# Kernel tuning notes

Hardware: AMD Instinct MI355X
Metric: run time of the kernel (lower is better)

## Reference

```python
import jax, jax.numpy as jnp
import numpy as np

N_NODES = 50000
N_EDGES = 800000


def _sage(x, src, dst, Wl, Wr, b, n):
    # PyG SAGEConv: lin_l(mean aggr of neighbors) + lin_r(x) (+ bias in lin_l)
    agg = jax.ops.segment_sum(x[src], dst, num_segments=n)
    cnt = jax.ops.segment_sum(jnp.ones((src.shape[0],), x.dtype), dst, num_segments=n)
    mean = agg / jnp.maximum(cnt, 1.0)[:, None]
    return mean @ Wl + x @ Wr + b


def _gat(x, src, dst, W, att_src, att_dst, b, n):
    H, C = att_src.shape
    h = (x @ W).reshape(n, H, C)                      # [N,H,C]
    a_s = jnp.sum(h * att_src, axis=-1)               # [N,H]
    a_d = jnp.sum(h * att_dst, axis=-1)               # [N,H]
    e = jax.nn.leaky_relu(a_s[src] + a_d[dst], 0.2)   # [E,H]
    m = jax.ops.segment_max(e, dst, num_segments=n)   # per-dst softmax (stable)
    ex = jnp.exp(e - m[dst])
    s = jax.ops.segment_sum(ex, dst, num_segments=n)
    alpha = ex / (s[dst] + 1e-16)                     # [E,H]
    out = jax.ops.segment_sum(h[src] * alpha[:, :, None], dst, num_segments=n)
    return out.reshape(n, H * C) + b


def setup_inputs() -> dict:
    key = jax.random.key(0)
    ks = jax.random.split(key, 16)
    F_IN, H1, GH, HEADS, H2, NC = 20, 256, 32, 4, 256, 5
    GOUT = GH * HEADS
    sc = 0.05
    return {
        "x": jax.random.normal(ks[0], (N_NODES, F_IN), jnp.float32),
        "edge_index": jax.random.randint(ks[1], (2, N_EDGES), 0, N_NODES, jnp.int32),
        "sage1_Wl": jax.random.normal(ks[2], (F_IN, H1), jnp.float32) * sc,
        "sage1_Wr": jax.random.normal(ks[3], (F_IN, H1), jnp.float32) * sc,
        "sage1_b": jnp.zeros((H1,), jnp.float32),
        "gat_W": jax.random.normal(ks[4], (H1, GOUT), jnp.float32) * sc,
        "gat_att_src": jax.random.normal(ks[5], (HEADS, GH), jnp.float32) * sc,
        "gat_att_dst": jax.random.normal(ks[6], (HEADS, GH), jnp.float32) * sc,
        "gat_b": jnp.zeros((GOUT,), jnp.float32),
        "sage2_Wl": jax.random.normal(ks[7], (GOUT, H2), jnp.float32) * sc,
        "sage2_Wr": jax.random.normal(ks[8], (GOUT, H2), jnp.float32) * sc,
        "sage2_b": jnp.zeros((H2,), jnp.float32),
        "cls_W": jax.random.normal(ks[9], (H2, NC), jnp.float32) * sc,
        "cls_b": jnp.zeros((NC,), jnp.float32),
    }


def reference(x, edge_index, sage1_Wl, sage1_Wr, sage1_b, gat_W, gat_att_src,
              gat_att_dst, gat_b, sage2_Wl, sage2_Wr, sage2_b, cls_W, cls_b):
    n = x.shape[0]
    src, dst = edge_index[0], edge_index[1]
    h = jax.nn.relu(_sage(x, src, dst, sage1_Wl, sage1_Wr, sage1_b, n))
    h = jax.nn.elu(_gat(h, src, dst, gat_W, gat_att_src, gat_att_dst, gat_b, n))
    h = jax.nn.relu(_sage(h, src, dst, sage2_Wl, sage2_Wr, sage2_b, n))
    return h @ cls_W + cls_b
```

## Files before the change

### kernel.cpp

```cpp
#include <hip/hip_runtime.h>
#include <math.h>

#define N_NODES 50000
#define N_EDGES 800000
#define TPB 256
#define NCHUNK ((N_NODES + 255) / 256)

typedef short s16x8 __attribute__((ext_vector_type(8)));
typedef float f32x4 __attribute__((ext_vector_type(4)));

__device__ __forceinline__ unsigned short f2bf(float f) {
    unsigned u = __float_as_uint(f);
    u += 0x7fffu + ((u >> 16) & 1u);
    return (unsigned short)(u >> 16);
}
__device__ __forceinline__ float bf2f(unsigned short h) {
    return __uint_as_float(((unsigned)h) << 16);
}

__global__ void wt_all_k(const float* __restrict__ s1Wl, const float* __restrict__ s1Wr,
                         const float* __restrict__ gW, const float* __restrict__ s2Wl,
                         const float* __restrict__ s2Wr, unsigned short* __restrict__ Wt1,
                         unsigned short* __restrict__ Wt2, unsigned short* __restrict__ Wt3) {
    int idx = blockIdx.x * TPB + threadIdx.x;
    if (idx < 16384) {
        int n = idx >> 6, k = idx & 63;
        float v = 0.f;
        if (k < 20) v = s1Wl[k * 256 + n];
        else if (k < 40) v = s1Wr[(k - 20) * 256 + n];
        Wt1[idx] = f2bf(v);
    } else if (idx < 49152) {
        int j = idx - 16384;
        int n = j >> 8, k = j & 255;
        Wt2[j] = f2bf(gW[(size_t)k * 128 + n]);
    } else if (idx < 114688) {
        int j = idx - 49152;
        int n = j >> 8, k = j & 255;
        float v = (k < 128) ? s2Wl[(size_t)k * 256 + n] : s2Wr[(size_t)(k - 128) * 256 + n];
        Wt3[j] = f2bf(v);
    }
}

template<int ACT, int OBF>
__global__ void gemm_mfma(const float* __restrict__ A1, int K1,
                          const float* __restrict__ A2, int K2,
                          const unsigned short* __restrict__ Wt, int Kp,
                          const float* __restrict__ bias,
                          float* __restrict__ out, unsigned short* __restrict__ outb,
                          int NO) {
    constexpr int BM = 128, BK = 32, LDP = 40;
    __shared__ unsigned short sA[BM * LDP];
    __shared__ unsigned short sB[128 * LDP];
    const int K = K1 + K2;
    const int T = Kp / BK;
    const int tid = threadIdx.x;
    const int lane = tid & 63, wid = tid >> 6;
    const int wr = wid >> 1, wc = wid & 1;
    const int row0 = blockIdx.y * BM, col0 = blockIdx.x * 128;
    const int l15 = lane & 15, l4 = lane >> 4;
    f32x4 acc[4][4] = {};

    for (int t = 0; t < T; ++t) {
        __syncthreads();
#pragma unroll
        for (int j = 0; j < 4; ++j) {
            int e = tid + j * 256;
            int r = e >> 3, k4 = e & 7;
            int kg = t * BK + k4 * 4, mg = row0 + r;
            float4 v = {0.f, 0.f, 0.f, 0.f};
            if (mg < N_NODES) {
                if (kg < K1)     v = *(const float4*)&A1[(size_t)mg * K1 + kg];
                else if (kg < K) v = *(const float4*)&A2[(size_t)mg * K2 + (kg - K1)];
            }
            ushort4 b;
            b.x = f2bf(v.x); b.y = f2bf(v.y); b.z = f2bf(v.z); b.w = f2bf(v.w);
            *(ushort4*)&sA[r * LDP + k4 * 4] = b;
        }
#pragma unroll
        for (int j = 0; j < 2; ++j) {
            int e = tid + j * 256;
            int n = e >> 2, k8 = e & 3;
            int4 v = *(const int4*)&Wt[(size_t)(col0 + n) * Kp + t * BK + k8 * 8];
            *(int4*)&sB[n * LDP + k8 * 8] = v;
        }
        __syncthreads();
        s16x8 af[4], bfr[4];
#pragma unroll
        for (int i = 0; i < 4; ++i) {
            af[i]  = *(const s16x8*)&sA[(wr * 64 + i * 16 + l15) * LDP + l4 * 8];
            bfr[i] = *(const s16x8*)&sB[(wc * 64 + i * 16 + l15) * LDP + l4 * 8];
        }
#pragma unroll
        for (int mi = 0; mi < 4; ++mi)
#pragma unroll
            for (int ni = 0; ni < 4; ++ni)
                acc[mi][ni] = __builtin_amdgcn_mfma_f32_16x16x32_bf16(
                    af[mi], bfr[ni], acc[mi][ni], 0, 0, 0);
    }
#pragma unroll
    for (int mi = 0; mi < 4; ++mi) {
#pragma unroll
        for (int ni = 0; ni < 4; ++ni) {
            int col = col0 + wc * 64 + ni * 16 + l15;
            float bb = bias ? bias[col] : 0.f;
#pragma unroll
            for (int r = 0; r < 4; ++r) {
                int row = row0 + wr * 64 + mi * 16 + l4 * 4 + r;
                if (row < N_NODES) {
                    float v = acc[mi][ni][r] + bb;
                    if (ACT) v = fmaxf(v, 0.f);
                    if (OBF) outb[(size_t)row * NO + col] = f2bf(v);
                    else     out[(size_t)row * NO + col] = v;
                }
            }
        }
    }
}

template<int ACT, int OBF>
__global__ void gemm_mfma_bf(const unsigned short* __restrict__ A1, int K1,
                             const unsigned short* __restrict__ A2, int K2,
                             const unsigned short* __restrict__ Wt, int Kp,
                             const float* __restrict__ bias,
                             float* __restrict__ out, unsigned short* __restrict__ outb,
                             int NO) {
    constexpr int BM = 128, BK = 32, LDP = 40;
    __shared__ unsigned short sA[BM * LDP];
    __shared__ unsigned short sB[128 * LDP];
    const int T = Kp / BK;
    const int tid = threadIdx.x;
    const int lane = tid & 63, wid = tid >> 6;
    const int wr = wid >> 1, wc = wid & 1;
    const int row0 = blockIdx.y * BM, col0 = blockIdx.x * 128;
    const int l15 = lane & 15, l4 = lane >> 4;
    f32x4 acc[4][4] = {};

    for (int t = 0; t < T; ++t) {
        __syncthreads();
#pragma unroll
        for (int j = 0; j < 2; ++j) {
            int e = tid + j * 256;
            int r = e >> 2, k8 = e & 3;
            int kg = t * BK + k8 * 8, mg = row0 + r;
            int4 v = {0, 0, 0, 0};
            if (mg < N_NODES) {
                if (kg < K1) v = *(const int4*)&A1[(size_t)mg * K1 + kg];
                else         v = *(const int4*)&A2[(size_t)mg * K2 + (kg - K1)];
            }
            *(int4*)&sA[r * LDP + k8 * 8] = v;
        }
#pragma unroll
        for (int j = 0; j < 2; ++j) {
            int e = tid + j * 256;
            int n = e >> 2, k8 = e & 3;
            int4 v = *(const int4*)&Wt[(size_t)(col0 + n) * Kp + t * BK + k8 * 8];
            *(int4*)&sB[n * LDP + k8 * 8] = v;
        }
        __syncthreads();
        s16x8 af[4], bfr[4];
#pragma unroll
        for (int i = 0; i < 4; ++i) {
            af[i]  = *(const s16x8*)&sA[(wr * 64 + i * 16 + l15) * LDP + l4 * 8];
            bfr[i] = *(const s16x8*)&sB[(wc * 64 + i * 16 + l15) * LDP + l4 * 8];
        }
#pragma unroll
        for (int mi = 0; mi < 4; ++mi)
#pragma unroll
            for (int ni = 0; ni < 4; ++ni)
                acc[mi][ni] = __builtin_amdgcn_mfma_f32_16x16x32_bf16(
                    af[mi], bfr[ni], acc[mi][ni], 0, 0, 0);
    }
#pragma unroll
    for (int mi = 0; mi < 4; ++mi) {
#pragma unroll
        for (int ni = 0; ni < 4; ++ni) {
            int col = col0 + wc * 64 + ni * 16 + l15;
            float bb = bias ? bias[col] : 0.f;
#pragma unroll
            for (int r = 0; r < 4; ++r) {
                int row = row0 + wr * 64 + mi * 16 + l4 * 4 + r;
                if (row < N_NODES) {
                    float v = acc[mi][ni][r] + bb;
                    if (ACT) v = fmaxf(v, 0.f);
                    if (OBF) outb[(size_t)row * NO + col] = f2bf(v);
                    else     out[(size_t)row * NO + col] = v;
                }
            }
        }
    }
}

__global__ void hist_k(const int* __restrict__ dst, int* __restrict__ deg) {
    int e = blockIdx.x * TPB + threadIdx.x;
    if (e < N_EDGES) atomicAdd(&deg[dst[e]], 1);
}

__global__ void scan1_k(const int* __restrict__ deg, int* __restrict__ rowptr,
                        int* __restrict__ bsum) {
    __shared__ int tmp[256];
    int tid = threadIdx.x;
    int idx = blockIdx.x * 256 + tid;
    int v = (idx < N_NODES) ? deg[idx] : 0;
    tmp[tid] = v;
    __syncthreads();
    for (int off = 1; off < 256; off <<= 1) {
        int t = (tid >= off) ? tmp[tid - off] : 0;
        __syncthreads();
        tmp[tid] += t;
        __syncthreads();
    }
    if (idx < N_NODES) rowptr[idx] = tmp[tid] - v;
    if (tid == 255) bsum[blockIdx.x] = tmp[255];
}

__global__ void scan2_k(int* __restrict__ bsum) {
    __shared__ int tmp[256];
    int tid = threadIdx.x;
    int v = (tid < NCHUNK) ? bsum[tid] : 0;
    tmp[tid] = v;
    __syncthreads();
    for (int off = 1; off < 256; off <<= 1) {
        int t = (tid >= off) ? tmp[tid - off] : 0;
        __syncthreads();
        tmp[tid] += t;
        __syncthreads();
    }
    if (tid < NCHUNK) bsum[tid] = tmp[tid] - v;
}

__global__ void scan3_k(int* __restrict__ rowptr, const int* __restrict__ bsum) {
    int idx = blockIdx.x * 256 + threadIdx.x;
    if (idx < N_NODES) rowptr[idx] += bsum[blockIdx.x];
    if (idx == 0) rowptr[N_NODES] = N_EDGES;
}

__global__ void fill_k(const int* __restrict__ src, const int* __restrict__ dst,
                       const int* __restrict__ rowptr, int* __restrict__ deg,
                       int* __restrict__ csr_src) {
    int e = blockIdx.x * TPB + threadIdx.x;
    if (e >= N_EDGES) return;
    int d = dst[e];
    int r = atomicSub(&deg[d], 1) - 1;
    csr_src[rowptr[d] + r] = src[e];
}

__global__ void gm20_k(const int* __restrict__ rowptr, const int* __restrict__ csr_src,
                       const float* __restrict__ feat, float* __restrict__ out) {
    int tid = threadIdx.x;
    int n = blockIdx.x * 8 + (tid >> 5);
    int c = tid & 31;
    if (n >= N_NODES || c >= 20) return;
    int e0 = rowptr[n], e1 = rowptr[n + 1];
    float acc = 0.f;
    int e = e0;
    for (; e + 1 < e1; e += 2) {
        acc += feat[(size_t)csr_src[e] * 20 + c] + feat[(size_t)csr_src[e + 1] * 20 + c];
    }
    if (e < e1) acc += feat[(size_t)csr_src[e] * 20 + c];
    out[(size_t)n * 20 + c] = acc / fmaxf((float)(e1 - e0), 1.0f);
}

__global__ void gather_mean_bf(const int* __restrict__ rowptr, const int* __restrict__ csr_src,
                               const unsigned short* __restrict__ featb,
                               unsigned short* __restrict__ outb) {
    int tid = threadIdx.x;
    int n = blockIdx.x * 8 + (tid >> 5);
    int c = tid & 31;
    int e0 = rowptr[n], e1 = rowptr[n + 1];
    float4 acc = {0.f, 0.f, 0.f, 0.f};
    int e = e0;
    for (; e + 3 < e1; e += 4) {
        int s0 = csr_src[e], s1 = csr_src[e + 1], s2 = csr_src[e + 2], s3 = csr_src[e + 3];
        ushort4 u0 = *(const ushort4*)&featb[(size_t)s0 * 128 + c * 4];
        ushort4 u1 = *(const ushort4*)&featb[(size_t)s1 * 128 + c * 4];
        ushort4 u2 = *(const ushort4*)&featb[(size_t)s2 * 128 + c * 4];
        ushort4 u3 = *(const ushort4*)&featb[(size_t)s3 * 128 + c * 4];
        acc.x += (bf2f(u0.x) + bf2f(u1.x)) + (bf2f(u2.x) + bf2f(u3.x));
        acc.y += (bf2f(u0.y) + bf2f(u1.y)) + (bf2f(u2.y) + bf2f(u3.y));
        acc.z += (bf2f(u0.z) + bf2f(u1.z)) + (bf2f(u2.z) + bf2f(u3.z));
        acc.w += (bf2f(u0.w) + bf2f(u1.w)) + (bf2f(u2.w) + bf2f(u3.w));
    }
    for (; e < e1; ++e) {
        ushort4 u = *(const ushort4*)&featb[(size_t)csr_src[e] * 128 + c * 4];
        acc.x += bf2f(u.x); acc.y += bf2f(u.y); acc.z += bf2f(u.z); acc.w += bf2f(u.w);
    }
    float inv = 1.0f / fmaxf((float)(e1 - e0), 1.0f);
    ushort4 o;
    o.x = f2bf(acc.x * inv); o.y = f2bf(acc.y * inv);
    o.z = f2bf(acc.z * inv); o.w = f2bf(acc.w * inv);
    *(ushort4*)&outb[(size_t)n * 128 + c * 4] = o;
}

__global__ void att_scores_bf(const unsigned short* __restrict__ hb,
                              const float* __restrict__ att_src,
                              const float* __restrict__ att_dst,
                              float* __restrict__ as_, float* __restrict__ ad_) {
    int idx = blockIdx.x * TPB + threadIdx.x;
    if (idx >= N_NODES * 4) return;
    int n = idx >> 2, hd = idx & 3;
    const unsigned short* row = hb + (size_t)n * 128 + hd * 32;
    float sa = 0.f, sd = 0.f;
#pragma unroll
    for (int c4 = 0; c4 < 8; ++c4) {
        ushort4 u = *(const ushort4*)&row[c4 * 4];
        const float* asr = &att_src[hd * 32 + c4 * 4];
        const float* adr = &att_dst[hd * 32 + c4 * 4];
        sa = fmaf(bf2f(u.x), asr[0], sa); sd = fmaf(bf2f(u.x), adr[0], sd);
        sa = fmaf(bf2f(u.y), asr[1], sa); sd = fmaf(bf2f(u.y), adr[1], sd);
        sa = fmaf(bf2f(u.z), asr[2], sa); sd = fmaf(bf2f(u.z), adr[2], sd);
        sa = fmaf(bf2f(u.w), asr[3], sa); sd = fmaf(bf2f(u.w), adr[3], sd);
    }
    as_[idx] = sa;
    ad_[idx] = sd;
}

__global__ void gat_gather_bf(const int* __restrict__ rowptr, const int* __restrict__ csr_src,
                              const unsigned short* __restrict__ hb,
                              const float* __restrict__ as_, const float* __restrict__ ad_,
                              const float* __restrict__ gb,
                              unsigned short* __restrict__ outb) {
    int tid = threadIdx.x;
    int n = blockIdx.x * 8 + (tid >> 5);
    int c = tid & 31;
    int hd = c >> 3;
    int e0 = rowptr[n], e1 = rowptr[n + 1];
    float ad = ad_[n * 4 + hd];
    float m = -INFINITY, s = 0.f;
    float4 acc = {0.f, 0.f, 0.f, 0.f};
    int e = e0;
    for (; e + 3 < e1; e += 4) {
        int s0 = csr_src[e], s1 = csr_src[e + 1], s2 = csr_src[e + 2], s3 = csr_src[e + 3];
        float a0 = as_[s0 * 4 + hd] + ad;
        float a1 = as_[s1 * 4 + hd] + ad;
        float a2 = as_[s2 * 4 + hd] + ad;
        float a3 = as_[s3 * 4 + hd] + ad;
        a0 = a0 >= 0.f ? a0 : 0.2f * a0;
        a1 = a1 >= 0.f ? a1 : 0.2f * a1;
        a2 = a2 >= 0.f ? a2 : 0.2f * a2;
        a3 = a3 >= 0.f ? a3 : 0.2f * a3;
        float pm = fmaxf(fmaxf(a0, a1), fmaxf(a2, a3));
        if (pm > m) {
            float sc = __expf(m - pm);
            s *= sc; acc.x *= sc; acc.y *= sc; acc.z *= sc; acc.w *= sc;
            m = pm;
        }
        float ex0 = __expf(a0 - m), ex1 = __expf(a1 - m);
        float ex2 = __expf(a2 - m), ex3 = __expf(a3 - m);
        s += (ex0 + ex1) + (ex2 + ex3);
        ushort4 u0 = *(const ushort4*)&hb[(size_t)s0 * 128 + c * 4];
        ushort4 u1 = *(const ushort4*)&hb[(size_t)s1 * 128 + c * 4];
        ushort4 u2 = *(const ushort4*)&hb[(size_t)s2 * 128 + c * 4];
        ushort4 u3 = *(const ushort4*)&hb[(size_t)s3 * 128 + c * 4];
        acc.x = fmaf(bf2f(u0.x), ex0, acc.x); acc.y = fmaf(bf2f(u0.y), ex0, acc.y);
        acc.z = fmaf(bf2f(u0.z), ex0, acc.z); acc.w = fmaf(bf2f(u0.w), ex0, acc.w);
        acc.x = fmaf(bf2f(u1.x), ex1, acc.x); acc.y = fmaf(bf2f(u1.y), ex1, acc.y);
        acc.z = fmaf(bf2f(u1.z), ex1, acc.z); acc.w = fmaf(bf2f(u1.w), ex1, acc.w);
        acc.x = fmaf(bf2f(u2.x), ex2, acc.x); acc.y = fmaf(bf2f(u2.y), ex2, acc.y);
        acc.z = fmaf(bf2f(u2.z), ex2, acc.z); acc.w = fmaf(bf2f(u2.w), ex2, acc.w);
        acc.x = fmaf(bf2f(u3.x), ex3, acc.x); acc.y = fmaf(bf2f(u3.y), ex3, acc.y);
        acc.z = fmaf(bf2f(u3.z), ex3, acc.z); acc.w = fmaf(bf2f(u3.w), ex3, acc.w);
    }
    for (; e < e1; ++e) {
        int s0 = csr_src[e];
        float a = as_[s0 * 4 + hd] + ad;
        a = a >= 0.f ? a : 0.2f * a;
        if (a > m) {
            float sc = __expf(m - a);
            s *= sc; acc.x *= sc; acc.y *= sc; acc.z *= sc; acc.w *= sc;
            m = a;
        }
        float ex = __expf(a - m);
        s += ex;
        ushort4 u = *(const ushort4*)&hb[(size_t)s0 * 128 + c * 4];
        acc.x = fmaf(bf2f(u.x), ex, acc.x); acc.y = fmaf(bf2f(u.y), ex, acc.y);
        acc.z = fmaf(bf2f(u.z), ex, acc.z); acc.w = fmaf(bf2f(u.w), ex, acc.w);
    }
    float inv = 1.0f / (s + 1e-16f);
    float rx = acc.x * inv + gb[c * 4 + 0];
    float ry = acc.y * inv + gb[c * 4 + 1];
    float rz = acc.z * inv + gb[c * 4 + 2];
    float rw = acc.w * inv + gb[c * 4 + 3];
    rx = rx > 0.f ? rx : expm1f(rx);
    ry = ry > 0.f ? ry : expm1f(ry);
    rz = rz > 0.f ? rz : expm1f(rz);
    rw = rw > 0.f ? rw : expm1f(rw);
    ushort4 o;
    o.x = f2bf(rx); o.y = f2bf(ry); o.z = f2bf(rz); o.w = f2bf(rw);
    *(ushort4*)&outb[(size_t)n * 128 + c * 4] = o;
}

__global__ void cls_k(const float* __restrict__ h, const float* __restrict__ W,
                      const float* __restrict__ b, float* __restrict__ out) {
    __shared__ float sW[256 * 5];
    for (int i = threadIdx.x; i < 1280; i += TPB) sW[i] = W[i];
    __syncthreads();
    int n = blockIdx.x * TPB + threadIdx.x;
    if (n >= N_NODES) return;
    const float4* row = (const float4*)(h + (size_t)n * 256);
    float acc[5] = {0.f, 0.f, 0.f, 0.f, 0.f};
    for (int k4 = 0; k4 < 64; ++k4) {
        float4 v = row[k4];
        const float* w = &sW[k4 * 4 * 5];
#pragma unroll
        for (int c = 0; c < 5; ++c) acc[c] = fmaf(v.x, w[c], acc[c]);
#pragma unroll
        for (int c = 0; c < 5; ++c) acc[c] = fmaf(v.y, w[5 + c], acc[c]);
#pragma unroll
        for (int c = 0; c < 5; ++c) acc[c] = fmaf(v.z, w[10 + c], acc[c]);
#pragma unroll
        for (int c = 0; c < 5; ++c) acc[c] = fmaf(v.w, w[15 + c], acc[c]);
    }
#pragma unroll
    for (int c = 0; c < 5; ++c) out[(size_t)n * 5 + c] = acc[c] + b[c];
}

extern "C" void kernel_launch(void* const* d_in, const int* in_sizes, int n_in,
                              void* d_out, int out_size, void* d_ws, size_t ws_size,
                              hipStream_t stream) {
    const float* x    = (const float*)d_in[0];
    const int*   ei   = (const int*)d_in[1];
    const float* s1Wl = (const float*)d_in[2];
    const float* s1Wr = (const float*)d_in[3];
    const float* s1b  = (const float*)d_in[4];
    const float* gW   = (const float*)d_in[5];
    const float* gas  = (const float*)d_in[6];
    const float* gad  = (const float*)d_in[7];
    const float* gb   = (const float*)d_in[8];
    const float* s2Wl = (const float*)d_in[9];
    const float* s2Wr = (const float*)d_in[10];
    const float* s2b  = (const float*)d_in[11];
    const float* clsW = (const float*)d_in[12];
    const float* clsb = (const float*)d_in[13];
    float* out = (float*)d_out;
    const int* src = ei;
    const int* dst = ei + N_EDGES;

    float* ws  = (float*)d_ws;
    float* A    = ws;
    float* M20  = A + (size_t)N_NODES * 256;
    float* as_  = M20 + (size_t)N_NODES * 20;
    float* ad_  = as_ + N_NODES * 4;
    int* deg     = (int*)(ad_ + N_NODES * 4);
    int* bsum    = deg + N_NODES;
    int* rowptr  = bsum + 256;
    int* csr_src = rowptr + N_NODES + 1;
    unsigned short* Wt1 = (unsigned short*)(csr_src + N_EDGES);
    unsigned short* Wt2 = Wt1 + 256 * 64;
    unsigned short* Wt3 = Wt2 + 128 * 256;
    unsigned short* Ab  = Wt3 + 256 * 256;
    unsigned short* Cb  = Ab + (size_t)N_NODES * 256;
    unsigned short* Db  = Cb + (size_t)N_NODES * 128;
    unsigned short* Mb  = Db + (size_t)N_NODES * 128;

    const int MB = (N_NODES + 127) / 128;

    wt_all_k<<<(114688 + TPB - 1) / TPB, TPB, 0, stream>>>(s1Wl, s1Wr, gW, s2Wl, s2Wr,
                                                           Wt1, Wt2, Wt3);

    hipMemsetAsync(deg, 0, N_NODES * sizeof(int), stream);
    hist_k<<<(N_EDGES + TPB - 1) / TPB, TPB, 0, stream>>>(dst, deg);
    scan1_k<<<NCHUNK, 256, 0, stream>>>(deg, rowptr, bsum);
    scan2_k<<<1, 256, 0, stream>>>(bsum);
    scan3_k<<<NCHUNK, 256, 0, stream>>>(rowptr, bsum);
    fill_k<<<(N_EDGES + TPB - 1) / TPB, TPB, 0, stream>>>(src, dst, rowptr, deg, csr_src);

    gm20_k<<<(N_NODES + 7) / 8, 256, 0, stream>>>(rowptr, csr_src, x, M20);
    gemm_mfma<1, 1><<<dim3(2, MB), 256, 0, stream>>>(M20, 20, x, 20, Wt1, 64, s1b,
                                                     nullptr, Ab, 256);

    gemm_mfma_bf<0, 1><<<dim3(1, MB), 256, 0, stream>>>(Ab, 256, nullptr, 0, Wt2, 256,
                                                        nullptr, nullptr, Cb, 128);
    att_scores_bf<<<(N_NODES * 4 + TPB - 1) / TPB, TPB, 0, stream>>>(Cb, gas, gad, as_, ad_);
    gat_gather_bf<<<N_NODES / 8, 256, 0, stream>>>(rowptr, csr_src, Cb, as_, ad_, gb, Db);

    gather_mean_bf<<<N_NODES / 8, 256, 0, stream>>>(rowptr, csr_src, Db, Mb);
    gemm_mfma_bf<1, 0><<<dim3(2, MB), 256, 0, stream>>>(Mb, 128, Db, 128, Wt3, 256, s2b,
                                                        A, nullptr, 256);

    cls_k<<<(N_NODES + TPB - 1) / TPB, TPB, 0, stream>>>(A, clsW, clsb, out);
}
```

Baseline: 296.0 us.

## Fuse classifier into final GEMM epilogue, widen gather batches, fold deg memset

The classifier matmul is folded into the epilogue of the last SAGE GEMM. Each column block reduces its ReLU outputs against the class weights in registers and shared memory, writes per-block partials, and a small combine kernel adds the bias. This removes the fp32 N×256 intermediate write and its re-read. The GAT gather now loads 8 edges per iteration, with lanes cooperatively computing scores and broadcasting them by shuffles. The mean gather is unrolled to 8 edges, and zeroing of deg moves into the weight-transpose kernel so the memset call goes away.

After: 299.2 us. No clear change (+1.1%).

```diff
diff --git a/kernel.cpp b/kernel.cpp
--- a/kernel.cpp
+++ b/kernel.cpp
@@ -21,8 +21,10 @@
 __global__ void wt_all_k(const float* __restrict__ s1Wl, const float* __restrict__ s1Wr,
                          const float* __restrict__ gW, const float* __restrict__ s2Wl,
                          const float* __restrict__ s2Wr, unsigned short* __restrict__ Wt1,
-                         unsigned short* __restrict__ Wt2, unsigned short* __restrict__ Wt3) {
+                         unsigned short* __restrict__ Wt2, unsigned short* __restrict__ Wt3,
+                         int* __restrict__ deg) {
     int idx = blockIdx.x * TPB + threadIdx.x;
+    if (idx < N_NODES) deg[idx] = 0;
     if (idx < 16384) {
         int n = idx >> 6, k = idx & 63;
         float v = 0.f;
@@ -41,13 +43,12 @@
     }
 }
 
-template<int ACT, int OBF>
+template<int ACT>
 __global__ void gemm_mfma(const float* __restrict__ A1, int K1,
                           const float* __restrict__ A2, int K2,
                           const unsigned short* __restrict__ Wt, int Kp,
                           const float* __restrict__ bias,
-                          float* __restrict__ out, unsigned short* __restrict__ outb,
-                          int NO) {
+                          unsigned short* __restrict__ outb, int NO) {
     constexpr int BM = 128, BK = 32, LDP = 40;
     __shared__ unsigned short sA[BM * LDP];
     __shared__ unsigned short sB[128 * LDP];
@@ -109,21 +110,20 @@
                 if (row < N_NODES) {
                     float v = acc[mi][ni][r] + bb;
                     if (ACT) v = fmaxf(v, 0.f);
-                    if (OBF) outb[(size_t)row * NO + col] = f2bf(v);
-                    else     out[(size_t)row * NO + col] = v;
+                    outb[(size_t)row * NO + col] = f2bf(v);
                 }
             }
         }
     }
 }
 
-template<int ACT, int OBF>
+template<int ACT, int CLS>
 __global__ void gemm_mfma_bf(const unsigned short* __restrict__ A1, int K1,
                              const unsigned short* __restrict__ A2, int K2,
                              const unsigned short* __restrict__ Wt, int Kp,
                              const float* __restrict__ bias,
-                             float* __restrict__ out, unsigned short* __restrict__ outb,
-                             int NO) {
+                             unsigned short* __restrict__ outb, int NO,
+                             const float* __restrict__ clsW, float* __restrict__ pp) {
     constexpr int BM = 128, BK = 32, LDP = 40;
     __shared__ unsigned short sA[BM * LDP];
     __shared__ unsigned short sB[128 * LDP];
@@ -170,24 +170,81 @@
                 acc[mi][ni] = __builtin_amdgcn_mfma_f32_16x16x32_bf16(
                     af[mi], bfr[ni], acc[mi][ni], 0, 0, 0);
     }
-#pragma unroll
-    for (int mi = 0; mi < 4; ++mi) {
-#pragma unroll
-        for (int ni = 0; ni < 4; ++ni) {
-            int col = col0 + wc * 64 + ni * 16 + l15;
-            float bb = bias ? bias[col] : 0.f;
-#pragma unroll
-            for (int r = 0; r < 4; ++r) {
-                int row = row0 + wr * 64 + mi * 16 + l4 * 4 + r;
-                if (row < N_NODES) {
-                    float v = acc[mi][ni][r] + bb;
-                    if (ACT) v = fmaxf(v, 0.f);
-                    if (OBF) outb[(size_t)row * NO + col] = f2bf(v);
-                    else     out[(size_t)row * NO + col] = v;
+
+    if (CLS == 0) {
+#pragma unroll
+        for (int mi = 0; mi < 4; ++mi) {
+#pragma unroll
+            for (int ni = 0; ni < 4; ++ni) {
+                int col = col0 + wc * 64 + ni * 16 + l15;
+                float bb = bias ? bias[col] : 0.f;
+#pragma unroll
+                for (int r = 0; r < 4; ++r) {
+                    int row = row0 + wr * 64 + mi * 16 + l4 * 4 + r;
+                    if (row < N_NODES) {
+                        float v = acc[mi][ni][r] + bb;
+                        if (ACT) v = fmaxf(v, 0.f);
+                        outb[(size_t)row * NO + col] = f2bf(v);
+                    }
                 }
             }
         }
-    }
+    } else {
+        __syncthreads();
+        float* sClsW = (float*)sA;
+        float* cp    = (float*)sB;
+        for (int i = tid; i < 640; i += 256)
+            sClsW[i] = clsW[(size_t)(col0 + i / 5) * 5 + (i % 5)];
+        __syncthreads();
+        float bcol[4];
+#pragma unroll
+        for (int ni = 0; ni < 4; ++ni)
+            bcol[ni] = bias[col0 + wc * 64 + ni * 16 + l15];
+#pragma unroll
+        for (int mi = 0; mi < 4; ++mi) {
+#pragma unroll
+            for (int r = 0; r < 4; ++r) {
+                float p0 = 0.f, p1 = 0.f, p2 = 0.f, p3 = 0.f, p4 = 0.f;
+#pragma unroll
+                for (int ni = 0; ni < 4; ++ni) {
+                    float v = fmaxf(acc[mi][ni][r] + bcol[ni], 0.f);
+                    const float* w = &sClsW[(wc * 64 + ni * 16 + l15) * 5];
+                    p0 = fmaf(v, w[0], p0); p1 = fmaf(v, w[1], p1);
+                    p2 = fmaf(v, w[2], p2); p3 = fmaf(v, w[3], p3);
+                    p4 = fmaf(v, w[4], p4);
+                }
+#pragma unroll
+                for (int msk = 1; msk < 16; msk <<= 1) {
+                    p0 += __shfl_xor(p0, msk, 16);
+                    p1 += __shfl_xor(p1, msk, 16);
+                    p2 += __shfl_xor(p2, msk, 16);
+                    p3 += __shfl_xor(p3, msk, 16);
+                    p4 += __shfl_xor(p4, msk, 16);
+                }
+                if (l15 == 0) {
+                    int rr = wr * 64 + mi * 16 + l4 * 4 + r;
+                    float* d = &cp[(wc * 128 + rr) * 5];
+                    d[0] = p0; d[1] = p1; d[2] = p2; d[3] = p3; d[4] = p4;
+                }
+            }
+        }
+        __syncthreads();
+        for (int i = tid; i < 640; i += 256) {
+            int rr = i / 5, cc = i - rr * 5;
+            int row = row0 + rr;
+            if (row < N_NODES)
+                pp[(size_t)blockIdx.x * ((size_t)N_NODES * 5) + (size_t)row * 5 + cc]
+                    = cp[rr * 5 + cc] + cp[(128 + rr) * 5 + cc];
+        }
+    }
+}
+
+__global__ void combine_k(const float* __restrict__ pp, const float* __restrict__ clsb,
+                          float* __restrict__ out) {
+    int idx = blockIdx.x * TPB + threadIdx.x;
+    if (idx >= N_NODES * 5) return;
+    int c = idx % 5;
+    out[idx] = pp[idx] + pp[(size_t)N_NODES * 5 + idx] + clsb[c];
 }
 
 __global__ void hist_k(const int* __restrict__ dst, int* __restrict__ deg) {
@@ -269,16 +326,16 @@
     int e0 = rowptr[n], e1 = rowptr[n + 1];
     float4 acc = {0.f, 0.f, 0.f, 0.f};
     int e = e0;
-    for (; e + 3 < e1; e += 4) {
-        int s0 = csr_src[e], s1 = csr_src[e + 1], s2 = csr_src[e + 2], s3 = csr_src[e + 3];
-        ushort4 u0 = *(const ushort4*)&featb[(size_t)s0 * 128 + c * 4];
-        ushort4 u1 = *(const ushort4*)&featb[(size_t)s1 * 128 + c * 4];
-        ushort4 u2 = *(const ushort4*)&featb[(size_t)s2 * 128 + c * 4];
-        ushort4 u3 = *(const ushort4*)&featb[(size_t)s3 * 128 + c * 4];
-        acc.x += (bf2f(u0.x) + bf2f(u1.x)) + (bf2f(u2.x) + bf2f(u3.x));
-        acc.y += (bf2f(u0.y) + bf2f(u1.y)) + (bf2f(u2.y) + bf2f(u3.y));
-        acc.z += (bf2f(u0.z) + bf2f(u1.z)) + (bf2f(u2.z) + bf2f(u3.z));
-        acc.w += (bf2f(u0.w) + bf2f(u1.w)) + (bf2f(u2.w) + bf2f(u3.w));
+    for (; e + 7 < e1; e += 8) {
+        ushort4 u[8];
+#pragma unroll
+        for (int j = 0; j < 8; ++j)
+            u[j] = *(const ushort4*)&featb[(size_t)csr_src[e + j] * 128 + c * 4];
+#pragma unroll
+        for (int j = 0; j < 8; ++j) {
+            acc.x += bf2f(u[j].x); acc.y += bf2f(u[j].y);
+            acc.z += bf2f(u[j].z); acc.w += bf2f(u[j].w);
+        }
     }
     for (; e < e1; ++e) {
         ushort4 u = *(const ushort4*)&featb[(size_t)csr_src[e] * 128 + c * 4];
@@ -323,42 +380,47 @@
     int n = blockIdx.x * 8 + (tid >> 5);
     int c = tid & 31;
     int hd = c >> 3;
+    int q = c & 7;
     int e0 = rowptr[n], e1 = rowptr[n + 1];
     float ad = ad_[n * 4 + hd];
     float m = -INFINITY, s = 0.f;
     float4 acc = {0.f, 0.f, 0.f, 0.f};
     int e = e0;
-    for (; e + 3 < e1; e += 4) {
-        int s0 = csr_src[e], s1 = csr_src[e + 1], s2 = csr_src[e + 2], s3 = csr_src[e + 3];
-        float a0 = as_[s0 * 4 + hd] + ad;
-        float a1 = as_[s1 * 4 + hd] + ad;
-        float a2 = as_[s2 * 4 + hd] + ad;
-        float a3 = as_[s3 * 4 + hd] + ad;
-        a0 = a0 >= 0.f ? a0 : 0.2f * a0;
-        a1 = a1 >= 0.f ? a1 : 0.2f * a1;
-        a2 = a2 >= 0.f ? a2 : 0.2f * a2;
-        a3 = a3 >= 0.f ? a3 : 0.2f * a3;
-        float pm = fmaxf(fmaxf(a0, a1), fmaxf(a2, a3));
+    for (; e + 7 < e1; e += 8) {
+        int sq = csr_src[e + q];
+        float aq = as_[sq * 4 + hd] + ad;
+        aq = aq >= 0.f ? aq : 0.2f * aq;
+        float pm = aq;
+        pm = fmaxf(pm, __shfl_xor(pm, 1, 8));
+        pm = fmaxf(pm, __shfl_xor(pm, 2, 8));
+        pm = fmaxf(pm, __shfl_xor(pm, 4, 8));
         if (pm > m) {
             float sc = __expf(m - pm);
             s *= sc; acc.x *= sc; acc.y *= sc; acc.z *= sc; acc.w *= sc;
             m = pm;
         }
-        float ex0 = __expf(a0 - m), ex1 = __expf(a1 - m);
-        float ex2 = __expf(a2 - m), ex3 = __expf(a3 - m);
-        s += (ex0 + ex1) + (ex2 + ex3);
-        ushort4 u0 = *(const ushort4*)&hb[(size_t)s0 * 128 + c * 4];
-        ushort4 u1 = *(const ushort4*)&hb[(size_t)s1 * 128 + c * 4];
-        ushort4 u2 = *(const ushort4*)&hb[(size_t)s2 * 128 + c * 4];
-        ushort4 u3 = *(const ushort4*)&hb[(size_t)s3 * 128 + c * 4];
-        acc.x = fmaf(bf2f(u0.x), ex0, acc.x); acc.y = fmaf(bf2f(u0.y), ex0, acc.y);
-        acc.z = fmaf(bf2f(u0.z), ex0, acc.z); acc.w = fmaf(bf2f(u0.w), ex0, acc.w);
-        acc.x = fmaf(bf2f(u1.x), ex1, acc.x); acc.y = fmaf(bf2f(u1.y), ex1, acc.y);
-        acc.z = fmaf(bf2f(u1.z), ex1, acc.z); acc.w = fmaf(bf2f(u1.w), ex1, acc.w);
-        acc.x = fmaf(bf2f(u2.x), ex2, acc.x); acc.y = fmaf(bf2f(u2.y), ex2, acc.y);
-        acc.z = fmaf(bf2f(u2.z), ex2, acc.z); acc.w = fmaf(bf2f(u2.w), ex2, acc.w);
-        acc.x = fmaf(bf2f(u3.x), ex3, acc.x); acc.y = fmaf(bf2f(u3.y), ex3, acc.y);
-        acc.z = fmaf(bf2f(u3.z), ex3, acc.z); acc.w = fmaf(bf2f(u3.w), ex3, acc.w);
+        float exq = __expf(aq - m);
+        float exs[8];
+        int   sj[8];
+#pragma unroll
+        for (int j = 0; j < 8; ++j) {
+            exs[j] = __shfl(exq, j, 8);
+            sj[j]  = __shfl(sq, j, 8);
+        }
+        s += ((exs[0] + exs[1]) + (exs[2] + exs[3]))
+           + ((exs[4] + exs[5]) + (exs[6] + exs[7]));
+        ushort4 u[8];
+#pragma unroll
+        for (int j = 0; j < 8; ++j)
+            u[j] = *(const ushort4*)&hb[(size_t)sj[j] * 128 + c * 4];
+#pragma unroll
+        for (int j = 0; j < 8; ++j) {
+            float ex = exs[j];
+            acc.x = fmaf(bf2f(u[j].x), ex, acc.x);
+            acc.y = fmaf(bf2f(u[j].y), ex, acc.y);
+            acc.z = fmaf(bf2f(u[j].z), ex, acc.z);
+            acc.w = fmaf(bf2f(u[j].w), ex, acc.w);
+        }
     }
     for (; e < e1; ++e) {
         int s0 = csr_src[e];
@@ -387,31 +449,6 @@
     ushort4 o;
     o.x = f2bf(rx); o.y = f2bf(ry); o.z = f2bf(rz); o.w = f2bf(rw);
     *(ushort4*)&outb[(size_t)n * 128 + c * 4] = o;
-}
-
-__global__ void cls_k(const float* __restrict__ h, const float* __restrict__ W,
-                      const float* __restrict__ b, float* __restrict__ out) {
-    __shared__ float sW[256 * 5];
-    for (int i = threadIdx.x; i < 1280; i += TPB) sW[i] = W[i];
-    __syncthreads();
-    int n = blockIdx.x * TPB + threadIdx.x;
-    if (n >= N_NODES) return;
-    const float4* row = (const float4*)(h + (size_t)n * 256);
-    float acc[5] = {0.f, 0.f, 0.f, 0.f, 0.f};
-    for (int k4 = 0; k4 < 64; ++k4) {
-        float4 v = row[k4];
-        const float* w = &sW[k4 * 4 * 5];
-#pragma unroll
-        for (int c = 0; c < 5; ++c) acc[c] = fmaf(v.x, w[c], acc[c]);
-#pragma unroll
-        for (int c = 0; c < 5; ++c) acc[c] = fmaf(v.y, w[5 + c], acc[c]);
-#pragma unroll
-        for (int c = 0; c < 5; ++c) acc[c] = fmaf(v.z, w[10 + c], acc[c]);
-#pragma unroll
-        for (int c = 0; c < 5; ++c) acc[c] = fmaf(v.w, w[15 + c], acc[c]);
-    }
-#pragma unroll
-    for (int c = 0; c < 5; ++c) out[(size_t)n * 5 + c] = acc[c] + b[c];
 }
 
 extern "C" void kernel_launch(void* const* d_in, const int* in_sizes, int n_in,
@@ -436,14 +473,14 @@
     const int* dst = ei + N_EDGES;
 
     float* ws  = (float*)d_ws;
-    float* A    = ws;
-    float* M20  = A + (size_t)N_NODES * 256;
+    float* M20  = ws;
     float* as_  = M20 + (size_t)N_NODES * 20;
     float* ad_  = as_ + N_NODES * 4;
-    int* deg     = (int*)(ad_ + N_NODES * 4);
+    float* pp   = ad_ + N_NODES * 4;
+    int* deg     = (int*)(pp + (size_t)2 * N_NODES * 5);
     int* bsum    = deg + N_NODES;
     int* rowptr  = bsum + 256;
-    int* csr_src = rowptr + N_NODES + 1;
+    int* csr_src = rowptr + N_NODES + 4;
     unsigned short* Wt1 = (unsigned short*)(csr_src + N_EDGES);
     unsigned short* Wt2 = Wt1 + 256 * 64;
     unsigned short* Wt3 = Wt2 + 128 * 256;
@@ -455,9 +492,8 @@
     const int MB = (N_NODES + 127) / 128;
 
     wt_all_k<<<(114688 + TPB - 1) / TPB, TPB, 0, stream>>>(s1Wl, s1Wr, gW, s2Wl, s2Wr,
-                                                           Wt1, Wt2, Wt3);
-
-    hipMemsetAsync(deg, 0, N_NODES * sizeof(int), stream);
+                                                           Wt1, Wt2, Wt3, deg);
+
     hist_k<<<(N_EDGES + TPB - 1) / TPB, TPB, 0, stream>>>(dst, deg);
     scan1_k<<<NCHUNK, 256, 0, stream>>>(deg, rowptr, bsum);
     scan2_k<<<1, 256, 0, stream>>>(bsum);
@@ -465,17 +501,16 @@
     fill_k<<<(N_EDGES + TPB - 1) / TPB, TPB, 0, stream>>>(src, dst, rowptr, deg, csr_src);
 
     gm20_k<<<(N_NODES + 7) / 8, 256, 0, stream>>>(rowptr, csr_src, x, M20);
-    gemm_mfma<1, 1><<<dim3(2, MB), 256, 0, stream>>>(M20, 20, x, 20, Wt1, 64, s1b,
-                                                     nullptr, Ab, 256);
-
-    gemm_mfma_bf<0, 1><<<dim3(1, MB), 256, 0, stream>>>(Ab, 256, nullptr, 0, Wt2, 256,
-                                                        nullptr, nullptr, Cb, 128);
+    gemm_mfma<1><<<dim3(2, MB), 256, 0, stream>>>(M20, 20, x, 20, Wt1, 64, s1b, Ab, 256);
+
+    gemm_mfma_bf<0, 0><<<dim3(1, MB), 256, 0, stream>>>(Ab, 256, nullptr, 0, Wt2, 256,
+                                                        nullptr, Cb, 128, nullptr, nullptr);
     att_scores_bf<<<(N_NODES * 4 + TPB - 1) / TPB, TPB, 0, stream>>>(Cb, gas, gad, as_, ad_);
     gat_gather_bf<<<N_NODES / 8, 256, 0, stream>>>(rowptr, csr_src, Cb, as_, ad_, gb, Db);
 
     gather_mean_bf<<<N_NODES / 8, 256, 0, stream>>>(rowptr, csr_src, Db, Mb);
-    gemm_mfma_bf<1, 0><<<dim3(2, MB), 256, 0, stream>>>(Mb, 128, Db, 128, Wt3, 256, s2b,
-                                                        A, nullptr, 256);
-
-    cls_k<<<(N_NODES + TPB - 1) / TPB, TPB, 0, stream>>>(A, clsW, clsb, out);
-}
+    gemm_mfma_bf<1, 1><<<dim3(2, MB), 256, 0, stream>>>(Mb, 128, Db, 128, Wt3, 256, s2b,
+                                                        nullptr, 256, clsW, pp);
+
+    combine_k<<<(N_NODES * 5 + TPB - 1) / TPB, TPB, 0, stream>>>(pp, clsb, out);
+}
```
